# Performance work log

Measured on AMD Instinct MI355X. Metric: run time of the kernel, lower is better.

## Reference

```python
import jax, jax.numpy as jnp
import numpy as np

B, D, C = 2048, 128, 100000
S, M = 64.0, 0.5
EPS = 1e-07


def setup_inputs() -> dict:
    key = jax.random.key(0)
    k1, k2, k3 = jax.random.split(key, 3)
    emb = jax.random.normal(k1, (B, D), dtype=jnp.float32)
    labels = jax.random.randint(k2, (B,), 0, C, dtype=jnp.int64)
    # xavier_uniform for W[D, C]: bound = sqrt(6/(D+C))
    bound = float(np.sqrt(6.0 / (D + C)))
    W = jax.random.uniform(k3, (D, C), dtype=jnp.float32, minval=-bound, maxval=bound)
    return {"emb": emb, "labels": labels, "W": W}


def reference(emb, labels, W):
    # normalize columns of W (dim=0), matching F.normalize(W, p=2, dim=0)
    Wn = W / jnp.maximum(jnp.linalg.norm(W, axis=0, keepdims=True), 1e-12)
    logits = emb @ Wn  # [B, C]
    rows = jnp.arange(logits.shape[0])
    tgt = logits[rows, labels]  # [B]
    tgt_margin = jnp.cos(jnp.arccos(jnp.clip(tgt, -1.0 + EPS, 1.0 - EPS)) + M)
    # one-hot blend == replace only the target column
    logits = logits.at[rows, labels].set(tgt_margin)
    logits = logits * S
    logp = jax.nn.log_softmax(logits, axis=-1)
    return -jnp.mean(logp[rows, labels])
```

## Files before the change

### kernel.cpp

```cpp
#include <hip/hip_runtime.h>
#include <math.h>

#define B_TOT    2048
#define D_DIM    128
#define C_TOT    100000
#define MARGIN   0.5f
#define EPS_C    1e-7f
#define LN2F     0.6931471805599453f
#define S_LOG2E  92.33248261689366f
#define MU_COEF  34.929f
#define MU_PAD   20.0f
#define E2SCALE  8388608.0f
#define E2HI     2.08e9f
#define SKIPTHR  687865856.0f

#define NCHUNK   250
#define GPC      25
#define PF       5
#define NFILL    5
#define NRBLK    8

#define PREP_A   1563
#define PREP_B   128
#define PREP_C   512

typedef __attribute__((ext_vector_type(8))) _Float16 f16x8;
typedef __attribute__((ext_vector_type(4))) float    f32x4;
typedef unsigned int u32;

#define EXP2(x) __builtin_amdgcn_exp2f(x)

__global__ __launch_bounds__(256) void prep_kernel(
    const float* __restrict__ W, const float* __restrict__ emb,
    const int* __restrict__ labels,
    _Float16* __restrict__ Whf, _Float16* __restrict__ Ahf,
    float2* __restrict__ tval2, float* __restrict__ mneg)
{
    __shared__ float tile[128 * 65];
    __shared__ float ssp[4][64];
    __shared__ float ivs[64];

    const int bx = blockIdx.x, tid = threadIdx.x;
    if (bx < PREP_A) {
        const int c0 = bx * 64;
#pragma unroll
        for (int i = 0; i < 8; ++i) {
            int flat = tid + i * 256;
            int d    = flat >> 4;
            int c4   = flat & 15;
            int c    = c0 + c4 * 4;
            float4 v = {0.f, 0.f, 0.f, 0.f};
            if (c < C_TOT) v = *(const float4*)&W[(size_t)d * C_TOT + c];
            tile[d * 65 + c4 * 4 + 0] = v.x;
            tile[d * 65 + c4 * 4 + 1] = v.y;
            tile[d * 65 + c4 * 4 + 2] = v.z;
            tile[d * 65 + c4 * 4 + 3] = v.w;
        }
        __syncthreads();
        const int cl = tid & 63;
        const int q  = tid >> 6;
        float ss = 0.f;
#pragma unroll
        for (int d = 0; d < 32; ++d) {
            float x = tile[(q * 32 + d) * 65 + cl];
            ss = fmaf(x, x, ss);
        }
        ssp[q][cl] = ss;
        __syncthreads();
        if (q == 0)
            ivs[cl] = 1.f / fmaxf(sqrtf(ssp[0][cl] + ssp[1][cl] +
                                        ssp[2][cl] + ssp[3][cl]), 1e-12f);
        __syncthreads();
        const int c = c0 + cl;
        if (c < C_TOT) {
            float iv = ivs[cl];
            int g = c >> 4, lc = c & 15;
            _Float16* base = Whf + ((size_t)g * 2048 + lc * 8 + q * 512);
#pragma unroll
            for (int lq = 0; lq < 4; ++lq) {
                f16x8 o;
#pragma unroll
                for (int h = 0; h < 8; ++h)
                    o[h] = (_Float16)(tile[(q * 32 + lq * 8 + h) * 65 + cl] * iv);
                *(f16x8*)(base + lq * 128) = o;
            }
        }
    } else if (bx < PREP_A + PREP_B) {
        int i = (bx - PREP_A) * 256 + tid;
        float4 a = ((const float4*)emb)[2 * i];
        float4 b = ((const float4*)emb)[2 * i + 1];
        f16x8 v;
        v[0] = (_Float16)(a.x * S_LOG2E); v[1] = (_Float16)(a.y * S_LOG2E);
        v[2] = (_Float16)(a.z * S_LOG2E); v[3] = (_Float16)(a.w * S_LOG2E);
        v[4] = (_Float16)(b.x * S_LOG2E); v[5] = (_Float16)(b.y * S_LOG2E);
        v[6] = (_Float16)(b.z * S_LOG2E); v[7] = (_Float16)(b.w * S_LOG2E);
        ((f16x8*)Ahf)[i] = v;
    } else {
        int row  = (bx - PREP_A - PREP_B) * 4 + (tid >> 6);
        int lane = tid & 63;
        int lab  = labels[row];
        float e0 = emb[row * D_DIM + lane];
        float e1 = emb[row * D_DIM + 64 + lane];
        float w0 = W[(size_t)lane * C_TOT + lab];
        float w1 = W[(size_t)(64 + lane) * C_TOT + lab];
        float dot = e0 * w0 + e1 * w1;
        float sw  = w0 * w0 + w1 * w1;
        float se  = e0 * e0 + e1 * e1;
#pragma unroll
        for (int off = 32; off > 0; off >>= 1) {
            dot += __shfl_down(dot, off, 64);
            sw  += __shfl_down(sw,  off, 64);
            se  += __shfl_down(se,  off, 64);
        }
        if (lane == 0) {
            float ivl  = 1.f / fmaxf(sqrtf(sw), 1e-12f);
            float tdot = dot * ivl;
            float tc   = fminf(fmaxf(tdot, -1.f + EPS_C), 1.f - EPS_C);
            float tm   = cosf(acosf(tc) + MARGIN);
            tval2[row] = make_float2(tdot * S_LOG2E, tm * S_LOG2E);
            mneg[row]  = -(MU_COEF * sqrtf(se) + MU_PAD);
        }
    }
}

__global__ __launch_bounds__(256) void gemm_lse(
    const _Float16* __restrict__ Ahf, const _Float16* __restrict__ Whf,
    const float* __restrict__ mneg, float* __restrict__ partial)
{
    __shared__ _Float16 lds[2][PF * 2048];

    const int b  = blockIdx.x;
    const int L  = (b & 7) * 250 + (b >> 3);
    const int chunk = L >> 3;
    const int rb    = L & 7;
    const int tid = threadIdx.x;
    const int w   = tid >> 6;
    const int l   = tid & 63;
    const int lc  = l & 15;
    const int lq  = l >> 4;
    const int r0  = rb * 256 + w * 64;

    f16x8 afrag[4][4];
#pragma unroll
    for (int rt = 0; rt < 4; ++rt)
#pragma unroll
        for (int t = 0; t < 4; ++t)
            afrag[rt][t] = *(const f16x8*)&Ahf[(size_t)(r0 + rt * 16 + lc) * D_DIM
                                               + t * 32 + lq * 8];

    float cr[16];
#pragma unroll
    for (int rt = 0; rt < 4; ++rt)
#pragma unroll
        for (int j = 0; j < 4; ++j)
            cr[rt * 4 + j] = (127.0f + mneg[r0 + rt * 16 + lq * 4 + j]) * E2SCALE;
    float crw = cr[0];
#pragma unroll
    for (int j = 1; j < 16; ++j) crw = fmaxf(crw, cr[j]);

    const char* bsrc = (const char*)(Whf + (size_t)chunk * GPC * 2048);

    auto stage = [&](int bb, int fill) {
        const char* sp = bsrc + (size_t)fill * (PF * 4096);
        char*       dp = (char*)&lds[bb][0];
#pragma unroll
        for (int idx = tid; idx < PF * 256; idx += 256)
            __builtin_amdgcn_global_load_lds(
                (const __attribute__((address_space(1))) u32*)(sp + (size_t)idx * 16),
                (__attribute__((address_space(3))) u32*)(dp + idx * 16),
                16, 0, 0);
    };

    float s[16];
#pragma unroll
    for (int j = 0; j < 16; ++j) s[j] = 0.f;
    const f32x4 zv = {0.f, 0.f, 0.f, 0.f};

    stage(0, 0);
    __syncthreads();

#pragma unroll 1
    for (int f = 0; f < NFILL; ++f) {
        if (f + 1 < NFILL) stage((f + 1) & 1, f + 1);
        const _Float16* bp = &lds[f & 1][0];
#pragma unroll
        for (int i = 0; i < PF; ++i) {
            f32x4 acc0, acc1, acc2, acc3;
            {
                f16x8 bf = *(const f16x8*)(bp + i * 2048 + l * 8);
                acc0 = __builtin_amdgcn_mfma_f32_16x16x32_f16(afrag[0][0], bf, zv, 0, 0, 0);
                acc1 = __builtin_amdgcn_mfma_f32_16x16x32_f16(afrag[1][0], bf, zv, 0, 0, 0);
                acc2 = __builtin_amdgcn_mfma_f32_16x16x32_f16(afrag[2][0], bf, zv, 0, 0, 0);
                acc3 = __builtin_amdgcn_mfma_f32_16x16x32_f16(afrag[3][0], bf, zv, 0, 0, 0);
            }
#pragma unroll
            for (int t = 1; t < 4; ++t) {
                f16x8 bf = *(const f16x8*)(bp + i * 2048 + t * 512 + l * 8);
                acc0 = __builtin_amdgcn_mfma_f32_16x16x32_f16(afrag[0][t], bf, acc0, 0, 0, 0);
                acc1 = __builtin_amdgcn_mfma_f32_16x16x32_f16(afrag[1][t], bf, acc1, 0, 0, 0);
                acc2 = __builtin_amdgcn_mfma_f32_16x16x32_f16(afrag[2][t], bf, acc2, 0, 0, 0);
                acc3 = __builtin_amdgcn_mfma_f32_16x16x32_f16(afrag[3][t], bf, acc3, 0, 0, 0);
            }
            float m01 = fmaxf(fmaxf(acc0[0], acc0[1]), acc0[2]);
            float m02 = fmaxf(fmaxf(acc0[3], acc1[0]), acc1[1]);
            float m03 = fmaxf(fmaxf(acc1[2], acc1[3]), acc2[0]);
            float m04 = fmaxf(fmaxf(acc2[1], acc2[2]), acc2[3]);
            float m05 = fmaxf(fmaxf(acc3[0], acc3[1]), acc3[2]);
            float mA  = fmaxf(fmaxf(m01, m02), m03);
            float mB  = fmaxf(fmaxf(m04, m05), acc3[3]);
            float kb  = fmaf(fmaxf(mA, mB), E2SCALE, crw);
            if (__any(kb >= SKIPTHR)) {
#pragma unroll
                for (int j = 0; j < 4; ++j) {
                    float k0 = fmaf(acc0[j], E2SCALE, cr[j]);
                    float k1 = fmaf(acc1[j], E2SCALE, cr[4 + j]);
                    float k2 = fmaf(acc2[j], E2SCALE, cr[8 + j]);
                    float k3 = fmaf(acc3[j], E2SCALE, cr[12 + j]);
                    k0 = fminf(fmaxf(k0, 0.f), E2HI);
                    k1 = fminf(fmaxf(k1, 0.f), E2HI);
                    k2 = fminf(fmaxf(k2, 0.f), E2HI);
                    k3 = fminf(fmaxf(k3, 0.f), E2HI);
                    s[j]      += __int_as_float((int)k0);
                    s[4 + j]  += __int_as_float((int)k1);
                    s[8 + j]  += __int_as_float((int)k2);
                    s[12 + j] += __int_as_float((int)k3);
                }
            }
        }
        __syncthreads();
    }

#pragma unroll
    for (int off = 1; off < 16; off <<= 1)
#pragma unroll
        for (int j = 0; j < 16; ++j) s[j] += __shfl_xor(s[j], off, 64);

    if (lc == 0) {
#pragma unroll
        for (int rt = 0; rt < 4; ++rt)
#pragma unroll
            for (int i = 0; i < 4; ++i) {
                int grow = r0 + rt * 16 + lq * 4 + i;
                partial[(size_t)chunk * B_TOT + grow] = s[rt * 4 + i];
            }
    }
}

__global__ __launch_bounds__(256) void finalize1(
    const float* __restrict__ partial, const float2* __restrict__ tval2,
    const float* __restrict__ mneg, float* __restrict__ blockpart)
{
    __shared__ float red[4];
    const int wv   = threadIdx.x >> 6;
    const int lane = threadIdx.x & 63;
    const int r    = blockIdx.x * 4 + wv;

    float S = 0.f;
#pragma unroll
    for (int j = 0; j < 4; ++j) {
        int k = lane + 64 * j;
        if (k < NCHUNK) S += partial[(size_t)k * B_TOT + r];
    }
#pragma unroll
    for (int off = 32; off > 0; off >>= 1) S += __shfl_down(S, off, 64);

    if (lane == 0) {
        float  mh = -mneg[r];
        float2 t  = tval2[r];
        S += EXP2(t.y - mh) - EXP2(t.x - mh);
        S  = fmaxf(S, 1e-30f);
        red[wv] = LN2F * (mh + log2f(S) - t.y);
    }
    __syncthreads();
    if (threadIdx.x == 0)
        blockpart[blockIdx.x] = red[0] + red[1] + red[2] + red[3];
}

__global__ __launch_bounds__(256) void finalize2(
    const float* __restrict__ blockpart, float* __restrict__ out)
{
    __shared__ float red[4];
    int tid = threadIdx.x;
    float v = blockpart[tid] + blockpart[tid + 256];
#pragma unroll
    for (int off = 32; off > 0; off >>= 1) v += __shfl_down(v, off, 64);
    int lane = tid & 63, wv = tid >> 6;
    if (lane == 0) red[wv] = v;
    __syncthreads();
    if (tid == 0)
        out[0] = (red[0] + red[1] + red[2] + red[3]) / (float)B_TOT;
}

extern "C" void kernel_launch(void* const* d_in, const int* in_sizes, int n_in,
                              void* d_out, int out_size, void* d_ws, size_t ws_size,
                              hipStream_t stream)
{
    const float* emb    = (const float*)d_in[0];
    const int*   labels = (const int*)  d_in[1];
    const float* W      = (const float*)d_in[2];

    char* p = (char*)d_ws;
    _Float16* Whf  = (_Float16*)p;
    p += ((size_t)C_TOT / 16 + 4) * 2048 * 2;
    _Float16* Ahf  = (_Float16*)p;  p += (size_t)B_TOT * D_DIM * 2;
    float2*   tv2  = (float2*)p;    p += (size_t)B_TOT * 8;
    float*    mneg = (float*)p;     p += (size_t)B_TOT * 4;
    float*    part = (float*)p;     p += (size_t)NCHUNK * B_TOT * 4;
    float*    bpar = (float*)p;
    float*    out  = (float*)d_out;

    hipLaunchKernelGGL(prep_kernel, dim3(PREP_A + PREP_B + PREP_C), dim3(256), 0, stream,
                       W, emb, labels, Whf, Ahf, tv2, mneg);
    hipLaunchKernelGGL(gemm_lse, dim3(NCHUNK * NRBLK), dim3(256), 0, stream,
                       Ahf, Whf, mneg, part);
    hipLaunchKernelGGL(finalize1, dim3(B_TOT / 4), dim3(256), 0, stream,
                       part, tv2, mneg, bpar);
    hipLaunchKernelGGL(finalize2, dim3(1), dim3(256), 0, stream,
                       bpar, out);
}
```

Before: 84.00 us.

## Replace double-buffered fills with a per-group ring buffer using vmcnt waits

Replaces the two-buffer, five-group staging of W tiles with a nine-slot LDS ring that keeps eight single-group global-to-LDS loads in flight. Each iteration waits with s_waitcnt vmcnt(7) plus a barrier and then issues the next group's load. Past the end of the chunk it issues harmless dummy loads into a spare slot so the vmcnt count stays constant. The aim is smoother, deeper memory overlap with finer-grained synchronization, at the cost of a barrier every group and reliance on hand-counted vmcnt being correct.

```diff
diff --git a/kernel.cpp b/kernel.cpp
--- a/kernel.cpp
+++ b/kernel.cpp
@@ -16,8 +16,8 @@
 
 #define NCHUNK   250
 #define GPC      25
-#define PF       5
-#define NFILL    5
+#define RDEPTH   8
+#define NSLOT    9
 #define NRBLK    8
 
 #define PREP_A   1563
@@ -127,7 +127,7 @@
     const _Float16* __restrict__ Ahf, const _Float16* __restrict__ Whf,
     const float* __restrict__ mneg, float* __restrict__ partial)
 {
-    __shared__ _Float16 lds[2][PF * 2048];
+    __shared__ _Float16 lds[(NSLOT + 1) * 2048];
 
     const int b  = blockIdx.x;
     const int L  = (b & 7) * 250 + (b >> 3);
@@ -160,15 +160,11 @@
 
     const char* bsrc = (const char*)(Whf + (size_t)chunk * GPC * 2048);
 
-    auto stage = [&](int bb, int fill) {
-        const char* sp = bsrc + (size_t)fill * (PF * 4096);
-        char*       dp = (char*)&lds[bb][0];
-#pragma unroll
-        for (int idx = tid; idx < PF * 256; idx += 256)
-            __builtin_amdgcn_global_load_lds(
-                (const __attribute__((address_space(1))) u32*)(sp + (size_t)idx * 16),
-                (__attribute__((address_space(3))) u32*)(dp + idx * 16),
-                16, 0, 0);
+    auto issue = [&](int slot, int g) {
+        __builtin_amdgcn_global_load_lds(
+            (const __attribute__((address_space(1))) u32*)(bsrc + (size_t)g * 4096 + tid * 16),
+            (__attribute__((address_space(3))) u32*)((char*)lds + slot * 4096 + tid * 16),
+            16, 0, 0);
     };
 
     float s[16];
@@ -176,58 +172,58 @@
     for (int j = 0; j < 16; ++j) s[j] = 0.f;
     const f32x4 zv = {0.f, 0.f, 0.f, 0.f};
 
-    stage(0, 0);
-    __syncthreads();
+#pragma unroll
+    for (int g = 0; g < RDEPTH; ++g) issue(g, g);
 
 #pragma unroll 1
-    for (int f = 0; f < NFILL; ++f) {
-        if (f + 1 < NFILL) stage((f + 1) & 1, f + 1);
-        const _Float16* bp = &lds[f & 1][0];
-#pragma unroll
-        for (int i = 0; i < PF; ++i) {
-            f32x4 acc0, acc1, acc2, acc3;
-            {
-                f16x8 bf = *(const f16x8*)(bp + i * 2048 + l * 8);
-                acc0 = __builtin_amdgcn_mfma_f32_16x16x32_f16(afrag[0][0], bf, zv, 0, 0, 0);
-                acc1 = __builtin_amdgcn_mfma_f32_16x16x32_f16(afrag[1][0], bf, zv, 0, 0, 0);
-                acc2 = __builtin_amdgcn_mfma_f32_16x16x32_f16(afrag[2][0], bf, zv, 0, 0, 0);
-                acc3 = __builtin_amdgcn_mfma_f32_16x16x32_f16(afrag[3][0], bf, zv, 0, 0, 0);
+    for (int g = 0; g < GPC; ++g) {
+        asm volatile("s_waitcnt vmcnt(7)" ::: "memory");
+        __builtin_amdgcn_s_barrier();
+        if (g + RDEPTH < GPC) issue((g + RDEPTH) % NSLOT, g + RDEPTH);
+        else                  issue(NSLOT, g + RDEPTH - GPC);
+
+        const _Float16* bp = lds + (g % NSLOT) * 2048;
+        f32x4 acc0, acc1, acc2, acc3;
+        {
+            f16x8 bf = *(const f16x8*)(bp + l * 8);
+            acc0 = __builtin_amdgcn_mfma_f32_16x16x32_f16(afrag[0][0], bf, zv, 0, 0, 0);
+            acc1 = __builtin_amdgcn_mfma_f32_16x16x32_f16(afrag[1][0], bf, zv, 0, 0, 0);
+            acc2 = __builtin_amdgcn_mfma_f32_16x16x32_f16(afrag[2][0], bf, zv, 0, 0, 0);
+            acc3 = __builtin_amdgcn_mfma_f32_16x16x32_f16(afrag[3][0], bf, zv, 0, 0, 0);
+        }
+#pragma unroll
+        for (int t = 1; t < 4; ++t) {
+            f16x8 bf = *(const f16x8*)(bp + t * 512 + l * 8);
+            acc0 = __builtin_amdgcn_mfma_f32_16x16x32_f16(afrag[0][t], bf, acc0, 0, 0, 0);
+            acc1 = __builtin_amdgcn_mfma_f32_16x16x32_f16(afrag[1][t], bf, acc1, 0, 0, 0);
+            acc2 = __builtin_amdgcn_mfma_f32_16x16x32_f16(afrag[2][t], bf, acc2, 0, 0, 0);
+            acc3 = __builtin_amdgcn_mfma_f32_16x16x32_f16(afrag[3][t], bf, acc3, 0, 0, 0);
+        }
+        float m01 = fmaxf(fmaxf(acc0[0], acc0[1]), acc0[2]);
+        float m02 = fmaxf(fmaxf(acc0[3], acc1[0]), acc1[1]);
+        float m03 = fmaxf(fmaxf(acc1[2], acc1[3]), acc2[0]);
+        float m04 = fmaxf(fmaxf(acc2[1], acc2[2]), acc2[3]);
+        float m05 = fmaxf(fmaxf(acc3[0], acc3[1]), acc3[2]);
+        float mA  = fmaxf(fmaxf(m01, m02), m03);
+        float mB  = fmaxf(fmaxf(m04, m05), acc3[3]);
+        float kb  = fmaf(fmaxf(mA, mB), E2SCALE, crw);
+        if (__any(kb >= SKIPTHR)) {
+#pragma unroll
+            for (int j = 0; j < 4; ++j) {
+                float k0 = fmaf(acc0[j], E2SCALE, cr[j]);
+                float k1 = fmaf(acc1[j], E2SCALE, cr[4 + j]);
+                float k2 = fmaf(acc2[j], E2SCALE, cr[8 + j]);
+                float k3 = fmaf(acc3[j], E2SCALE, cr[12 + j]);
+                k0 = fminf(fmaxf(k0, 0.f), E2HI);
+                k1 = fminf(fmaxf(k1, 0.f), E2HI);
+                k2 = fminf(fmaxf(k2, 0.f), E2HI);
+                k3 = fminf(fmaxf(k3, 0.f), E2HI);
+                s[j]      += __int_as_float((int)k0);
+                s[4 + j]  += __int_as_float((int)k1);
+                s[8 + j]  += __int_as_float((int)k2);
+                s[12 + j] += __int_as_float((int)k3);
             }
-#pragma unroll
-            for (int t = 1; t < 4; ++t) {
-                f16x8 bf = *(const f16x8*)(bp + i * 2048 + t * 512 + l * 8);
-                acc0 = __builtin_amdgcn_mfma_f32_16x16x32_f16(afrag[0][t], bf, acc0, 0, 0, 0);
-                acc1 = __builtin_amdgcn_mfma_f32_16x16x32_f16(afrag[1][t], bf, acc1, 0, 0, 0);
-                acc2 = __builtin_amdgcn_mfma_f32_16x16x32_f16(afrag[2][t], bf, acc2, 0, 0, 0);
-                acc3 = __builtin_amdgcn_mfma_f32_16x16x32_f16(afrag[3][t], bf, acc3, 0, 0, 0);
-            }
-            float m01 = fmaxf(fmaxf(acc0[0], acc0[1]), acc0[2]);
-            float m02 = fmaxf(fmaxf(acc0[3], acc1[0]), acc1[1]);
-            float m03 = fmaxf(fmaxf(acc1[2], acc1[3]), acc2[0]);
-            float m04 = fmaxf(fmaxf(acc2[1], acc2[2]), acc2[3]);
-            float m05 = fmaxf(fmaxf(acc3[0], acc3[1]), acc3[2]);
-            float mA  = fmaxf(fmaxf(m01, m02), m03);
-            float mB  = fmaxf(fmaxf(m04, m05), acc3[3]);
-            float kb  = fmaf(fmaxf(mA, mB), E2SCALE, crw);
-            if (__any(kb >= SKIPTHR)) {
-#pragma unroll
-                for (int j = 0; j < 4; ++j) {
-                    float k0 = fmaf(acc0[j], E2SCALE, cr[j]);
-                    float k1 = fmaf(acc1[j], E2SCALE, cr[4 + j]);
-                    float k2 = fmaf(acc2[j], E2SCALE, cr[8 + j]);
-                    float k3 = fmaf(acc3[j], E2SCALE, cr[12 + j]);
-                    k0 = fminf(fmaxf(k0, 0.f), E2HI);
-                    k1 = fminf(fmaxf(k1, 0.f), E2HI);
-                    k2 = fminf(fmaxf(k2, 0.f), E2HI);
-                    k3 = fminf(fmaxf(k3, 0.f), E2HI);
-                    s[j]      += __int_as_float((int)k0);
-                    s[4 + j]  += __int_as_float((int)k1);
-                    s[8 + j]  += __int_as_float((int)k2);
-                    s[12 + j] += __int_as_float((int)k3);
-                }
-            }
-        }
-        __syncthreads();
+        }
     }
 
 #pragma unroll
```

Result: slower. 88.45 us (+5.3%).
